# Performance work log

Measured on AMD Instinct MI355X. Metric: run time of the kernel, lower is better.

The kernel has to match this reference:

```python
import jax, jax.numpy as jnp
import numpy as np

D_MODEL = 768
N_HEADS = 12
D_HEAD = 64
WINDOW = 16
LOOK_BACK = 1
IGNORE = -1.0e6


def look_around(x, backward=LOOK_BACK, forward=0, pad_value=0):
    # x: (b, n_windows, w, ...) -> (b, n_windows, w*(backward+forward+1), ...)
    n = x.shape[1]
    pad = [(0, 0)] * x.ndim
    pad[1] = (backward, forward)
    px = jnp.pad(x, pad, constant_values=pad_value)
    return jnp.concatenate([px[:, i:i + n] for i in range(backward + forward + 1)], axis=2)


def setup_inputs() -> dict:
    key = jax.random.key(0)
    k1, k2, k3 = jax.random.split(key, 3)
    B, T = 2, 2048
    x = jax.random.normal(k1, (B, T, D_MODEL), dtype=jnp.float32)
    W_abcde = jax.random.normal(k2, (D_MODEL, 5 * N_HEADS * D_HEAD), dtype=jnp.float32) * (1.0 / np.sqrt(D_MODEL))
    b_abcde = jnp.zeros((5 * N_HEADS * D_HEAD,), dtype=jnp.float32)
    W_O = jax.random.normal(k3, (N_HEADS * D_HEAD, D_MODEL), dtype=jnp.float32) * (1.0 / np.sqrt(N_HEADS * D_HEAD))
    b_O = jnp.zeros((D_MODEL,), dtype=jnp.float32)
    return {"x": x, "W_abcde": W_abcde, "b_abcde": b_abcde, "W_O": W_O, "b_O": b_O}


def reference(x, W_abcde, b_abcde, W_O, b_O):
    B, T, _ = x.shape
    w = WINDOW
    nw = T // w
    Ww = w * (LOOK_BACK + 1)  # look-around window length

    abcde = x @ W_abcde + b_abcde                                    # (B,T,5*H*D)
    abcde = abcde.reshape(B, T, 5, N_HEADS, D_HEAD).transpose(2, 0, 3, 1, 4)  # (5,B,H,T,D)
    a, b, c, d, e = [t.reshape(B * N_HEADS, nw, w, D_HEAD) for t in abcde]
    a_l, b_l, d_l, e_l = (look_around(t) for t in (a, b, d, e))       # (BH,nw,Ww,D)

    # causal mask, same construction as get_causal_mask (pad_value=0)
    seq = jnp.arange(T).reshape(1, nw, w)
    bb = look_around(seq)                                            # (1,nw,Ww)
    # mask[n,m,l] = (seq_n < bb_l) | (bb_l <= bb_m)
    mask = (seq[..., :, None, None] < bb[..., None, None, :]) | (bb[..., None, None, :] <= bb[..., None, :, None])

    # third-order attention scores: (BH, nw, w, Ww, Ww)
    scores = jnp.einsum('bnwd,bnmd,bnld->bnwml', c, a_l, b_l)
    scores = jnp.where(mask, IGNORE, scores)
    scores = jnp.where(scores == 0, IGNORE, scores)
    probs = jax.nn.softmax((scores / D_HEAD).reshape(B * N_HEADS, nw, w, Ww * Ww), axis=-1)
    probs = probs.reshape(scores.shape)

    z = jnp.einsum('bnwml,bnmd->bnwd', probs, d_l) + jnp.einsum('bnwml,bnld->bnwd', probs, e_l)
    z = z.reshape(B, N_HEADS, nw, w, D_HEAD).transpose(0, 2, 3, 1, 4).reshape(B, T, N_HEADS * D_HEAD)
    return z @ W_O + b_O
```

## Files before the change

kernel.cpp:

```cpp
#include <hip/hip_runtime.h>

#define T_SEQ   2048
#define NHEADS  12
#define DHEAD   64
#define WIN     16
#define WW      32
#define NWIN    128
#define DMODEL  768
#define NABCDE  3840
#define IGNORE_V (-1.0e6f)
#define PAD_K   72
#define L2E64   0.022542110013890053f

typedef float f32x4 __attribute__((ext_vector_type(4)));
typedef float f32x2 __attribute__((ext_vector_type(2)));
typedef short bf16x8 __attribute__((ext_vector_type(8)));

__device__ __forceinline__ short f2bf(float f) {
    unsigned u = __float_as_uint(f);
    unsigned r = (u + 0x7FFF + ((u >> 16) & 1)) >> 16;
    return (short)r;
}

__device__ __forceinline__ void gload_lds16(const short* g, short* l) {
    __builtin_amdgcn_global_load_lds(
        (const __attribute__((address_space(1))) void*)g,
        (__attribute__((address_space(3))) void*)l,
        16, 0, 0);
}

__global__ __launch_bounds__(256) void prep_kernel(
    const float* __restrict__ x, const float* __restrict__ W_abcde,
    const float* __restrict__ W_O,
    short* __restrict__ xb, short* __restrict__ Wt, short* __restrict__ WOt)
{
    __shared__ float tile[32][33];
    const int blk = blockIdx.x;
    const int tid = threadIdx.x;

    if (blk < 1536) {
        int i = (blk * 256 + tid) * 8;
        float4 a = *reinterpret_cast<const float4*>(&x[i]);
        float4 b = *reinterpret_cast<const float4*>(&x[i + 4]);
        union { short s[8]; uint4 u; } r;
        r.s[0] = f2bf(a.x); r.s[1] = f2bf(a.y); r.s[2] = f2bf(a.z); r.s[3] = f2bf(a.w);
        r.s[4] = f2bf(b.x); r.s[5] = f2bf(b.y); r.s[6] = f2bf(b.z); r.s[7] = f2bf(b.w);
        *reinterpret_cast<uint4*>(&xb[i]) = r.u;
        return;
    }
    const float* W; short* Wo; int N, bx, by;
    if (blk < 4416) {
        int t = blk - 1536;
        W = W_abcde; Wo = Wt; N = NABCDE;
        bx = (t % 120) * 32; by = (t / 120) * 32;
    } else {
        int t = blk - 4416;
        W = W_O; Wo = WOt; N = DMODEL;
        bx = (t % 24) * 32; by = (t / 24) * 32;
    }
    const int tx = tid & 31, ty = tid >> 5;
#pragma unroll
    for (int r = 0; r < 32; r += 8)
        tile[ty + r][tx] = W[(size_t)(by + ty + r) * N + bx + tx];
    __syncthreads();
#pragma unroll
    for (int r = 0; r < 32; r += 8)
        Wo[(size_t)(bx + ty + r) * DMODEL + by + tx] = f2bf(tile[tx][ty + r]);
}

__global__ __launch_bounds__(256) void gemm1_kernel(
    const short* __restrict__ A, const short* __restrict__ Bt,
    const float* __restrict__ bias, short* __restrict__ C,
    int M, int N, int K)
{
    __shared__ short As[2][128 * 32];
    __shared__ short Bs[2][64 * 32];

    const int tid  = threadIdx.x;
    const int wave = tid >> 6;
    const int lane = tid & 63;

    int bid = blockIdx.x;
    int xcd = bid & 7, t = bid >> 3;
    int sid = (t / 80) * 8 + xcd;
    int inner = t % 80;
    int sy = sid / 6, sn = sid - sy * 6;
    const int bm = (sy * 8 + (inner & 7)) * 128;
    const int bn = (sn * 10 + (inner >> 3)) * 64;

    const int st_row = lane >> 2;
    const int st_col = (lane & 3) * 8;
    const int fr_m = lane & 15;
    const int fr_k = (lane >> 4) * 8;
    const int wm = wave * 32;
    const int lc = lane & 15;
    const int ko = lane >> 4;

    const short* gsrc[6];
    short* ldst[6];
#pragma unroll
    for (int j = 0; j < 6; ++j) {
        int c = wave * 6 + j;
        if (c < 16) {
            int kt = c >> 3, rg = c & 7;
            gsrc[j] = A + (size_t)(bm + rg * 16 + st_row) * K + kt * 32 + st_col;
            ldst[j] = &As[kt][(rg * 16) * 32];
        } else {
            int cb = c - 16;
            int kt = cb >> 2, rg = cb & 3;
            gsrc[j] = Bt + (size_t)(bn + rg * 16 + st_row) * K + kt * 32 + st_col;
            ldst[j] = &Bs[kt][(rg * 16) * 32];
        }
    }

    f32x4 acc[2][4];
#pragma unroll
    for (int mi = 0; mi < 2; ++mi)
#pragma unroll
        for (int ni = 0; ni < 4; ++ni) acc[mi][ni] = (f32x4){0.f, 0.f, 0.f, 0.f};

    for (int k0 = 0; k0 < K; k0 += 64) {
#pragma unroll
        for (int j = 0; j < 6; ++j) gload_lds16(gsrc[j] + k0, ldst[j]);
        __syncthreads();

#pragma unroll
        for (int kt = 0; kt < 2; ++kt) {
            bf16x8 af[2], bf[4];
#pragma unroll
            for (int mi = 0; mi < 2; ++mi)
                af[mi] = *reinterpret_cast<const bf16x8*>(
                    &As[kt][(wm + mi * 16 + fr_m) * 32 + fr_k]);
#pragma unroll
            for (int ni = 0; ni < 4; ++ni)
                bf[ni] = *reinterpret_cast<const bf16x8*>(
                    &Bs[kt][(ni * 16 + fr_m) * 32 + fr_k]);
#pragma unroll
            for (int mi = 0; mi < 2; ++mi)
#pragma unroll
                for (int ni = 0; ni < 4; ++ni)
                    acc[mi][ni] = __builtin_amdgcn_mfma_f32_16x16x32_bf16(
                        af[mi], bf[ni], acc[mi][ni], 0, 0, 0);
        }
        __syncthreads();
    }

    float bv[4];
#pragma unroll
    for (int ni = 0; ni < 4; ++ni)
        bv[ni] = bias[bn + ni * 16 + lc];

    short* cb = &As[0][0];
#pragma unroll
    for (int mi = 0; mi < 2; ++mi) {
#pragma unroll
        for (int r = 0; r < 4; ++r) {
            int row = wm + mi * 16 + ko * 4 + r;
#pragma unroll
            for (int ni = 0; ni < 4; ++ni)
                cb[row * 64 + ni * 16 + lc] = f2bf(acc[mi][ni][r] + bv[ni]);
        }
    }
    __syncthreads();
#pragma unroll
    for (int q = 0; q < 4; ++q) {
        int f = tid + q * 256;
        int row = f >> 3, c16 = (f & 7) * 8;
        *reinterpret_cast<uint4*>(&C[(size_t)(bm + row) * N + bn + c16]) =
            *reinterpret_cast<const uint4*>(&cb[row * 64 + c16]);
    }
}

__global__ __launch_bounds__(256) void gemm_bf16_64(
    const short* __restrict__ A, const short* __restrict__ Bt,
    const float* __restrict__ bias, float* __restrict__ C,
    int M, int N, int K)
{
    __shared__ short As[2][64 * 32];
    __shared__ short Bs[2][64 * 32];

    const int tid  = threadIdx.x;
    const int wave = tid >> 6;
    const int lane = tid & 63;
    const int bm = blockIdx.y * 64;
    const int bn = blockIdx.x * 64;

    const int st_row = lane >> 2;
    const int st_col = (lane & 3) * 8;
    const int fr_m = lane & 15;
    const int fr_k = (lane >> 4) * 8;
    const int wm = wave * 16;

    const short* gsrc[4];
    short* ldst[4];
#pragma unroll
    for (int j = 0; j < 4; ++j) {
        int c = wave * 4 + j;
        if (c < 8) {
            int kt = c >> 2, rg = c & 3;
            gsrc[j] = A + (size_t)(bm + rg * 16 + st_row) * K + kt * 32 + st_col;
            ldst[j] = &As[kt][(rg * 16) * 32];
        } else {
            int cb = c - 8;
            int kt = cb >> 2, rg = cb & 3;
            gsrc[j] = Bt + (size_t)(bn + rg * 16 + st_row) * K + kt * 32 + st_col;
            ldst[j] = &Bs[kt][(rg * 16) * 32];
        }
    }

    f32x4 acc[4];
#pragma unroll
    for (int ni = 0; ni < 4; ++ni) acc[ni] = (f32x4){0.f, 0.f, 0.f, 0.f};

    for (int k0 = 0; k0 < K; k0 += 64) {
#pragma unroll
        for (int j = 0; j < 4; ++j) gload_lds16(gsrc[j] + k0, ldst[j]);
        __syncthreads();

#pragma unroll
        for (int kt = 0; kt < 2; ++kt) {
            bf16x8 af = *reinterpret_cast<const bf16x8*>(
                &As[kt][(wm + fr_m) * 32 + fr_k]);
#pragma unroll
            for (int ni = 0; ni < 4; ++ni) {
                bf16x8 bf = *reinterpret_cast<const bf16x8*>(
                    &Bs[kt][(ni * 16 + fr_m) * 32 + fr_k]);
                acc[ni] = __builtin_amdgcn_mfma_f32_16x16x32_bf16(
                    af, bf, acc[ni], 0, 0, 0);
            }
        }
        __syncthreads();
    }

    float bv[4];
#pragma unroll
    for (int ni = 0; ni < 4; ++ni)
        bv[ni] = bias[bn + ni * 16 + (lane & 15)];
    int rbase = bm + wm + (lane >> 4) * 4;
#pragma unroll
    for (int r = 0; r < 4; ++r) {
        size_t off = (size_t)(rbase + r) * N + bn + (lane & 15);
#pragma unroll
        for (int ni = 0; ni < 4; ++ni)
            C[off + ni * 16] = acc[ni][r] + bv[ni];
    }
}

__global__ __launch_bounds__(256) void attn_kernel(
    const short* __restrict__ abcde, short* __restrict__ z)
{
    const int blk = blockIdx.x;
    const int n  = blk & (NWIN - 1);
    const int bh = blk >> 7;
    const int b  = bh / NHEADS;
    const int h  = bh % NHEADS;

    __shared__ short sc[WIN * PAD_K];
    __shared__ short sa[WW * PAD_K];
    __shared__ short sb[WW * PAD_K];
    __shared__ short sd[WW * PAD_K];
    __shared__ short se[WW * PAD_K];
    __shared__ short epA[WIN * PAD_K];
    __shared__ float sinv[WIN];

    const int tid = threadIdx.x;
    const size_t rowbase = ((size_t)b * T_SEQ) * NABCDE;
    const int hd = h * DHEAD;

    if (tid < 128) {
        int row = tid >> 3, ch = (tid & 7) * 8;
        *reinterpret_cast<uint4*>(&sc[row * PAD_K + ch]) =
            *reinterpret_cast<const uint4*>(
                &abcde[rowbase + (size_t)(n * WIN + row) * NABCDE + 2 * DMODEL + hd + ch]);
    }
    {
        int row = tid >> 3, ch = (tid & 7) * 8;
        int t = n * WIN - WIN + row;
        uint4 va = {0u, 0u, 0u, 0u}, vb = va, vd = va, ve = va;
        if (t >= 0) {
            size_t base = rowbase + (size_t)t * NABCDE + hd + ch;
            va = *reinterpret_cast<const uint4*>(&abcde[base + 0 * DMODEL]);
            vb = *reinterpret_cast<const uint4*>(&abcde[base + 1 * DMODEL]);
            vd = *reinterpret_cast<const uint4*>(&abcde[base + 3 * DMODEL]);
            ve = *reinterpret_cast<const uint4*>(&abcde[base + 4 * DMODEL]);
        }
        *reinterpret_cast<uint4*>(&sa[row * PAD_K + ch]) = va;
        *reinterpret_cast<uint4*>(&sb[row * PAD_K + ch]) = vb;
        *reinterpret_cast<uint4*>(&sd[row * PAD_K + ch]) = vd;
        *reinterpret_cast<uint4*>(&se[row * PAD_K + ch]) = ve;
    }
    __syncthreads();

    const int wv = tid >> 6;
    const int lane = tid & 63;
    const int lc = lane & 15;
    const int ko = lane >> 4;

    f32x2 c2[2][4];
    bf16x8 bfrag[2][2];
#pragma unroll
    for (int kt = 0; kt < 2; ++kt) {
        union { bf16x8 v; unsigned u[4]; } Cf;
        Cf.v = *reinterpret_cast<const bf16x8*>(
            &sc[(wv * 4 + (lc & 3)) * PAD_K + kt * 32 + ko * 8]);
#pragma unroll
        for (int j = 0; j < 4; ++j) {
            c2[kt][j] = (f32x2){__uint_as_float(Cf.u[j] << 16),
                                __uint_as_float(Cf.u[j] & 0xffff0000u)};
        }
        bfrag[0][kt] = *reinterpret_cast<const bf16x8*>(&sb[lc * PAD_K + kt * 32 + ko * 8]);
        bfrag[1][kt] = *reinterpret_cast<const bf16x8*>(&sb[(16 + lc) * PAD_K + kt * 32 + ko * 8]);
    }

    f32x4 acc[8][2];
#pragma unroll
    for (int mt = 0; mt < 8; ++mt) {
        acc[mt][0] = (f32x4){0.f, 0.f, 0.f, 0.f};
        acc[mt][1] = (f32x4){0.f, 0.f, 0.f, 0.f};
    }
    __builtin_amdgcn_s_setprio(1);
#pragma unroll
    for (int mt = 0; mt < 8; ++mt) {
#pragma unroll
        for (int kt = 0; kt < 2; ++kt) {
            union { bf16x8 v; unsigned u[4]; } Ar, Rf;
            Ar.v = *reinterpret_cast<const bf16x8*>(
                &sa[(mt * 4 + (lc >> 2)) * PAD_K + kt * 32 + ko * 8]);
#pragma unroll
            for (int j = 0; j < 4; ++j) {
                f32x2 y = (f32x2){__uint_as_float(Ar.u[j] << 16),
                                  __uint_as_float(Ar.u[j] & 0xffff0000u)};
                f32x2 p = c2[kt][j] * y;
                Rf.u[j] = __builtin_amdgcn_perm(
                    __float_as_uint(p[1]), __float_as_uint(p[0]), 0x07060302);
            }
            acc[mt][0] = __builtin_amdgcn_mfma_f32_16x16x32_bf16(Rf.v, bfrag[0][kt], acc[mt][0], 0, 0, 0);
            acc[mt][1] = __builtin_amdgcn_mfma_f32_16x16x32_bf16(Rf.v, bfrag[1][kt], acc[mt][1], 0, 0, 0);
        }
    }
    __builtin_amdgcn_s_setprio(0);

    const int nbase = n * WIN;
    if (n != 0) {
#pragma unroll
        for (int lt = 0; lt < 2; ++lt) {
            const int l = lt * 16 + lc;
#pragma unroll
            for (int mt = 0; mt < 8; ++mt) {
                const bool mgt = l > (mt * 4 + ko);
#pragma unroll
                for (int reg = 0; reg < 4; ++reg) {
                    const bool keep = mgt && (wv * 4 + reg + WIN >= l);
                    float p = __builtin_amdgcn_exp2f(acc[mt][lt][reg] * L2E64);
                    acc[mt][lt][reg] = keep ? p : 0.0f;
                }
            }
        }
    } else {
        int bbl_h[2]; bool keepL[2][4];
#pragma unroll
        for (int lt = 0; lt < 2; ++lt) {
            int l = lt * 16 + lc;
            bbl_h[lt] = (l < WIN) ? 0 : (l - WIN);
#pragma unroll
            for (int reg = 0; reg < 4; ++reg)
                keepL[lt][reg] = (wv * 4 + reg) >= bbl_h[lt];
        }
#pragma unroll
        for (int mt = 0; mt < 8; ++mt) {
            int m = mt * 4 + ko;
            int bbm = (m < WIN) ? 0 : (m - WIN);
#pragma unroll
            for (int lt = 0; lt < 2; ++lt) {
                bool mgt = bbl_h[lt] > bbm;
#pragma unroll
                for (int reg = 0; reg < 4; ++reg) {
                    float s = acc[mt][lt][reg];
                    if (!(keepL[lt][reg] && mgt) || s == 0.0f)
                        acc[mt][lt][reg] = IGNORE_V;
                }
            }
        }
        float mx[4] = {-3.4e38f, -3.4e38f, -3.4e38f, -3.4e38f};
#pragma unroll
        for (int mt = 0; mt < 8; ++mt)
#pragma unroll
            for (int lt = 0; lt < 2; ++lt)
#pragma unroll
                for (int reg = 0; reg < 4; ++reg)
                    mx[reg] = fmaxf(mx[reg], acc[mt][lt][reg]);
#pragma unroll
        for (int reg = 0; reg < 4; ++reg) {
#pragma unroll
            for (int off = 1; off < 64; off <<= 1)
                mx[reg] = fmaxf(mx[reg], __shfl_xor(mx[reg], off, 64));
        }
        float c0[4];
#pragma unroll
        for (int reg = 0; reg < 4; ++reg) c0[reg] = -mx[reg] * L2E64;
#pragma unroll
        for (int mt = 0; mt < 8; ++mt)
#pragma unroll
            for (int lt = 0; lt < 2; ++lt)
#pragma unroll
                for (int reg = 0; reg < 4; ++reg)
                    acc[mt][lt][reg] = __builtin_amdgcn_exp2f(
                        fmaf(acc[mt][lt][reg], L2E64, c0[reg]));
    }

    float plv[2][4];
#pragma unroll
    for (int lt = 0; lt < 2; ++lt) {
#pragma unroll
        for (int reg = 0; reg < 4; ++reg) {
            float p = acc[0][lt][reg];
#pragma unroll
            for (int mt = 1; mt < 8; ++mt) p += acc[mt][lt][reg];
            p += __shfl_xor(p, 16, 64);
            p += __shfl_xor(p, 32, 64);
            plv[lt][reg] = p;
        }
        float w  = (ko & 1) ? plv[lt][1] : plv[lt][0];
        float w2 = (ko & 1) ? plv[lt][3] : plv[lt][2];
        float ww = (ko & 2) ? w2 : w;
        epA[(wv * 4 + ko) * PAD_K + 32 + lt * 16 + lc] = f2bf(ww);
    }

    {
        float s[4];
#pragma unroll
        for (int reg = 0; reg < 4; ++reg) {
            float t = plv[0][reg] + plv[1][reg];
            t += __shfl_xor(t, 1, 64);
            t += __shfl_xor(t, 2, 64);
            t += __shfl_xor(t, 4, 64);
            t += __shfl_xor(t, 8, 64);
            s[reg] = t;
        }
        if (lane == 0) {
#pragma unroll
            for (int reg = 0; reg < 4; ++reg) sinv[wv * 4 + reg] = 1.0f / s[reg];
        }
    }

    {
        float v8[8][4];
#pragma unroll
        for (int mt = 0; mt < 8; ++mt)
#pragma unroll
            for (int reg = 0; reg < 4; ++reg)
                v8[mt][reg] = acc[mt][0][reg] + acc[mt][1][reg];

        const bool s0 = lane & 1, s1 = lane & 2, s2 = lane & 4, s3 = lane & 8;
        float r1[4][4];
#pragma unroll
        for (int m2 = 0; m2 < 4; ++m2)
#pragma unroll
            for (int reg = 0; reg < 4; ++reg) {
                float u = v8[2 * m2][reg], w = v8[2 * m2 + 1][reg];
                float a = s0 ? w : u;
                float s = s0 ? u : w;
                r1[m2][reg] = a + __shfl_xor(s, 1, 64);
            }
        float r2[2][4];
#pragma unroll
        for (int m4 = 0; m4 < 2; ++m4)
#pragma unroll
            for (int reg = 0; reg < 4; ++reg) {
                float u = r1[2 * m4][reg], w = r1[2 * m4 + 1][reg];
                float a = s1 ? w : u;
                float s = s1 ? u : w;
                r2[m4][reg] = a + __shfl_xor(s, 2, 64);
            }
        float r3[4];
#pragma unroll
        for (int reg = 0; reg < 4; ++reg) {
            float u = r2[0][reg], w = r2[1][reg];
            float a = s2 ? w : u;
            float s = s2 ? u : w;
            r3[reg] = a + __shfl_xor(s, 4, 64);
        }
        float a0 = s3 ? r3[1] : r3[0];
        float q0 = s3 ? r3[0] : r3[1];
        float g0 = a0 + __shfl_xor(q0, 8, 64);
        float a1 = s3 ? r3[3] : r3[2];
        float q1 = s3 ? r3[2] : r3[3];
        float g1 = a1 + __shfl_xor(q1, 8, 64);

        int mcol = (lc & 7) * 4 + ko;
        int ib = wv * 4 + (lc >> 3);
        epA[ib * PAD_K + mcol]       = f2bf(g0);
        epA[(ib + 2) * PAD_K + mcol] = f2bf(g1);
    }

    const int dd = wv * 16 + lc;
    bf16x8 bd, be;
    {
        unsigned dv[8], ev[8];
#pragma unroll
        for (int j = 0; j < 8; ++j) {
            dv[j] = *reinterpret_cast<const unsigned short*>(&sd[(ko * 8 + j) * PAD_K + dd]);
            ev[j] = *reinterpret_cast<const unsigned short*>(&se[(ko * 8 + j) * PAD_K + dd]);
        }
        union { unsigned u[4]; bf16x8 v; } td, te;
#pragma unroll
        for (int j = 0; j < 4; ++j) {
            td.u[j] = __builtin_amdgcn_perm(dv[2 * j + 1], dv[2 * j], 0x05040100);
            te.u[j] = __builtin_amdgcn_perm(ev[2 * j + 1], ev[2 * j], 0x05040100);
        }
        bd = td.v; be = te.v;
    }
    __syncthreads();

    bf16x8 apm = *reinterpret_cast<const bf16x8*>(&epA[lc * PAD_K + ko * 8]);
    bf16x8 apl = *reinterpret_cast<const bf16x8*>(&epA[lc * PAD_K + 32 + ko * 8]);
    f32x4 zacc = (f32x4){0.f, 0.f, 0.f, 0.f};
    __builtin_amdgcn_s_setprio(1);
    zacc = __builtin_amdgcn_mfma_f32_16x16x32_bf16(apm, bd, zacc, 0, 0, 0);
    zacc = __builtin_amdgcn_mfma_f32_16x16x32_bf16(apl, be, zacc, 0, 0, 0);
    __builtin_amdgcn_s_setprio(0);

    short* zs = sd;
#pragma unroll
    for (int reg = 0; reg < 4; ++reg) {
        int i = ko * 4 + reg;
        zs[i * 64 + dd] = f2bf(zacc[reg] * sinv[i]);
    }
    __syncthreads();
    {
        int row = tid >> 4;
        int ch  = (tid & 15) * 4;
        *reinterpret_cast<uint2*>(
            &z[((size_t)b * T_SEQ + nbase + row) * (NHEADS * DHEAD) + hd + ch]) =
            *reinterpret_cast<const uint2*>(&zs[row * 64 + ch]);
    }
}

extern "C" void kernel_launch(void* const* d_in, const int* in_sizes, int n_in,
                              void* d_out, int out_size, void* d_ws, size_t ws_size,
                              hipStream_t stream) {
    const float* x        = (const float*)d_in[0];
    const float* W_abcde  = (const float*)d_in[1];
    const float* b_abcde  = (const float*)d_in[2];
    const float* W_O      = (const float*)d_in[3];
    const float* b_O      = (const float*)d_in[4];
    float* out = (float*)d_out;

    char* ws = (char*)d_ws;
    short* abcde = (short*)ws;
    short* xb    = (short*)(ws + (size_t)31457280);
    short* Wt    = (short*)(ws + (size_t)31457280 + 6291456);
    short* WOt   = (short*)(ws + (size_t)31457280 + 6291456 + 5898240);
    short* zb    = xb;

    const int M = 2 * T_SEQ;

    prep_kernel<<<dim3(4992), dim3(256), 0, stream>>>(
        x, W_abcde, W_O, xb, Wt, WOt);

    gemm1_kernel<<<dim3(1920), dim3(256), 0, stream>>>(
        xb, Wt, b_abcde, abcde, M, NABCDE, DMODEL);

    attn_kernel<<<dim3(2 * NHEADS * NWIN), dim3(256), 0, stream>>>(abcde, zb);

    gemm_bf16_64<<<dim3(DMODEL / 64, M / 64), dim3(256), 0, stream>>>(
        zb, WOt, b_O, out, M, DMODEL, DMODEL);
}
```

Measured before the change: 158.9 us.

## Enlarge QKV GEMM tile to 128x128 and prescale softmax constant into C operand

The first projection GEMM moves from 128x64 to 128x128 block tiles. Each wave now computes a 64x64 sub-tile, which raises MFMA work per LDS load and halves the grid to 960 blocks. The epilogue is staged in two halves through shared memory so it fits the existing buffer. Separately, the attention kernel folds the log2(e)/64 scale into the C fragment once, which removes a multiply per exponent in the masked softmax paths. The ignore constant is rescaled to match. Risks are fewer blocks for occupancy and tail balance, and higher register pressure.

Measured after the change: 158.5 us. Within noise of the previous version (-0.3%).

```diff
diff --git a/kernel.cpp b/kernel.cpp
--- a/kernel.cpp
+++ b/kernel.cpp
@@ -11,6 +11,7 @@
 #define IGNORE_V (-1.0e6f)
 #define PAD_K   72
 #define L2E64   0.022542110013890053f
+#define IGN_SC  (-22542.110013890053f)
 
 typedef float f32x4 __attribute__((ext_vector_type(4)));
 typedef float f32x2 __attribute__((ext_vector_type(2)));
@@ -74,7 +75,7 @@
     int M, int N, int K)
 {
     __shared__ short As[2][128 * 32];
-    __shared__ short Bs[2][64 * 32];
+    __shared__ short Bs[2][128 * 32];
 
     const int tid  = threadIdx.x;
     const int wave = tid >> 6;
@@ -82,65 +83,68 @@
 
     int bid = blockIdx.x;
     int xcd = bid & 7, t = bid >> 3;
-    int sid = (t / 80) * 8 + xcd;
-    int inner = t % 80;
-    int sy = sid / 6, sn = sid - sy * 6;
-    const int bm = (sy * 8 + (inner & 7)) * 128;
-    const int bn = (sn * 10 + (inner >> 3)) * 64;
+    int sidx = t / 40, inner = t % 40;
+    int sid = sidx * 8 + xcd;
+    int sy = sid / 3, sx = sid % 3;
+    const int ty = sy * 4 + (inner & 3);
+    const int tx = sx * 10 + (inner >> 2);
+    const int bm = ty * 128;
+    const int bn = tx * 128;
 
     const int st_row = lane >> 2;
     const int st_col = (lane & 3) * 8;
     const int fr_m = lane & 15;
     const int fr_k = (lane >> 4) * 8;
-    const int wm = wave * 32;
-    const int lc = lane & 15;
-    const int ko = lane >> 4;
-
-    const short* gsrc[6];
-    short* ldst[6];
-#pragma unroll
-    for (int j = 0; j < 6; ++j) {
-        int c = wave * 6 + j;
+    const int ko   = lane >> 4;
+    const int wr = wave >> 1;
+    const int wm = wr * 64;
+    const int wn = (wave & 1) * 64;
+
+    const short* gsrc[8];
+    short* ldst[8];
+#pragma unroll
+    for (int j = 0; j < 8; ++j) {
+        int c = wave * 8 + j;
         if (c < 16) {
             int kt = c >> 3, rg = c & 7;
             gsrc[j] = A + (size_t)(bm + rg * 16 + st_row) * K + kt * 32 + st_col;
             ldst[j] = &As[kt][(rg * 16) * 32];
         } else {
             int cb = c - 16;
-            int kt = cb >> 2, rg = cb & 3;
+            int kt = cb >> 3, rg = cb & 7;
             gsrc[j] = Bt + (size_t)(bn + rg * 16 + st_row) * K + kt * 32 + st_col;
             ldst[j] = &Bs[kt][(rg * 16) * 32];
         }
     }
 
-    f32x4 acc[2][4];
-#pragma unroll
-    for (int mi = 0; mi < 2; ++mi)
+    f32x4 acc[4][4];
+#pragma unroll
+    for (int mi = 0; mi < 4; ++mi)
 #pragma unroll
         for (int ni = 0; ni < 4; ++ni) acc[mi][ni] = (f32x4){0.f, 0.f, 0.f, 0.f};
 
     for (int k0 = 0; k0 < K; k0 += 64) {
 #pragma unroll
-        for (int j = 0; j < 6; ++j) gload_lds16(gsrc[j] + k0, ldst[j]);
+        for (int j = 0; j < 8; ++j) gload_lds16(gsrc[j] + k0, ldst[j]);
         __syncthreads();
 
 #pragma unroll
         for (int kt = 0; kt < 2; ++kt) {
-            bf16x8 af[2], bf[4];
-#pragma unroll
-            for (int mi = 0; mi < 2; ++mi)
+            bf16x8 af[4], bfv[4];
+#pragma unroll
+            for (int mi = 0; mi < 4; ++mi)
                 af[mi] = *reinterpret_cast<const bf16x8*>(
                     &As[kt][(wm + mi * 16 + fr_m) * 32 + fr_k]);
 #pragma unroll
             for (int ni = 0; ni < 4; ++ni)
-                bf[ni] = *reinterpret_cast<const bf16x8*>(
-                    &Bs[kt][(ni * 16 + fr_m) * 32 + fr_k]);
-#pragma unroll
-            for (int mi = 0; mi < 2; ++mi)
+                bfv[ni] = *reinterpret_cast<const bf16x8*>(
+                    &Bs[kt][(wn + ni * 16 + fr_m) * 32 + fr_k]);
+#pragma unroll
+            for (int mi = 0; mi < 4; ++mi)
 #pragma unroll
                 for (int ni = 0; ni < 4; ++ni)
                     acc[mi][ni] = __builtin_amdgcn_mfma_f32_16x16x32_bf16(
-                        af[mi], bf[ni], acc[mi][ni], 0, 0, 0);
+                        af[mi], bfv[ni], acc[mi][ni], 0, 0, 0);
         }
         __syncthreads();
     }
@@ -148,26 +152,34 @@
     float bv[4];
 #pragma unroll
     for (int ni = 0; ni < 4; ++ni)
-        bv[ni] = bias[bn + ni * 16 + lc];
+        bv[ni] = bias[bn + wn + ni * 16 + fr_m];
 
     short* cb = &As[0][0];
 #pragma unroll
-    for (int mi = 0; mi < 2; ++mi) {
-#pragma unroll
-        for (int r = 0; r < 4; ++r) {
-            int row = wm + mi * 16 + ko * 4 + r;
-#pragma unroll
-            for (int ni = 0; ni < 4; ++ni)
-                cb[row * 64 + ni * 16 + lc] = f2bf(acc[mi][ni][r] + bv[ni]);
-        }
-    }
-    __syncthreads();
-#pragma unroll
-    for (int q = 0; q < 4; ++q) {
-        int f = tid + q * 256;
-        int row = f >> 3, c16 = (f & 7) * 8;
-        *reinterpret_cast<uint4*>(&C[(size_t)(bm + row) * N + bn + c16]) =
-            *reinterpret_cast<const uint4*>(&cb[row * 64 + c16]);
+    for (int half = 0; half < 2; ++half) {
+        if (wr == half) {
+#pragma unroll
+            for (int mi = 0; mi < 4; ++mi) {
+#pragma unroll
+                for (int r = 0; r < 4; ++r) {
+                    int row = mi * 16 + ko * 4 + r;
+#pragma unroll
+                    for (int ni = 0; ni < 4; ++ni)
+                        cb[row * 128 + wn + ni * 16 + fr_m] =
+                            f2bf(acc[mi][ni][r] + bv[ni]);
+                }
+            }
+        }
+        __syncthreads();
+#pragma unroll
+        for (int q = 0; q < 4; ++q) {
+            int f = tid + q * 256;
+            int row = f >> 4, c16 = (f & 15) * 8;
+            *reinterpret_cast<uint4*>(
+                &C[(size_t)(bm + half * 64 + row) * N + bn + c16]) =
+                *reinterpret_cast<const uint4*>(&cb[row * 128 + c16]);
+        }
+        __syncthreads();
     }
 }
 
@@ -306,7 +318,8 @@
 #pragma unroll
         for (int j = 0; j < 4; ++j) {
             c2[kt][j] = (f32x2){__uint_as_float(Cf.u[j] << 16),
-                                __uint_as_float(Cf.u[j] & 0xffff0000u)};
+                                __uint_as_float(Cf.u[j] & 0xffff0000u)}
+                        * (f32x2){L2E64, L2E64};
         }
         bfrag[0][kt] = *reinterpret_cast<const bf16x8*>(&sb[lc * PAD_K + kt * 32 + ko * 8]);
         bfrag[1][kt] = *reinterpret_cast<const bf16x8*>(&sb[(16 + lc) * PAD_K + kt * 32 + ko * 8]);
@@ -351,7 +364,7 @@
 #pragma unroll
                 for (int reg = 0; reg < 4; ++reg) {
                     const bool keep = mgt && (wv * 4 + reg + WIN >= l);
-                    float p = __builtin_amdgcn_exp2f(acc[mt][lt][reg] * L2E64);
+                    float p = __builtin_amdgcn_exp2f(acc[mt][lt][reg]);
                     acc[mt][lt][reg] = keep ? p : 0.0f;
                 }
             }
@@ -377,7 +390,7 @@
                 for (int reg = 0; reg < 4; ++reg) {
                     float s = acc[mt][lt][reg];
                     if (!(keepL[lt][reg] && mgt) || s == 0.0f)
-                        acc[mt][lt][reg] = IGNORE_V;
+                        acc[mt][lt][reg] = IGN_SC;
                 }
             }
         }
@@ -395,9 +408,6 @@
             for (int off = 1; off < 64; off <<= 1)
                 mx[reg] = fmaxf(mx[reg], __shfl_xor(mx[reg], off, 64));
         }
-        float c0[4];
-#pragma unroll
-        for (int reg = 0; reg < 4; ++reg) c0[reg] = -mx[reg] * L2E64;
 #pragma unroll
         for (int mt = 0; mt < 8; ++mt)
 #pragma unroll
@@ -405,7 +415,7 @@
 #pragma unroll
                 for (int reg = 0; reg < 4; ++reg)
                     acc[mt][lt][reg] = __builtin_amdgcn_exp2f(
-                        fmaf(acc[mt][lt][reg], L2E64, c0[reg]));
+                        acc[mt][lt][reg] - mx[reg]);
     }
 
     float plv[2][4];
@@ -558,7 +568,7 @@
     prep_kernel<<<dim3(4992), dim3(256), 0, stream>>>(
         x, W_abcde, W_O, xb, Wt, WOt);
 
-    gemm1_kernel<<<dim3(1920), dim3(256), 0, stream>>>(
+    gemm1_kernel<<<dim3(960), dim3(256), 0, stream>>>(
         xb, Wt, b_abcde, abcde, M, NABCDE, DMODEL);
 
     attn_kernel<<<dim3(2 * NHEADS * NWIN), dim3(256), 0, stream>>>(abcde, zb);
```
